# Kernel tuning notes

Hardware: AMD Instinct MI355X
Metric: run time of the kernel (lower is better)

## Reference

```python
import jax, jax.numpy as jnp
import numpy as np

RBF_CO = 10.077141124806595


def setup_inputs() -> dict:
    key = jax.random.key(0)
    k1, k2, k3 = jax.random.split(key, 3)
    n, dim = 2048, 128
    N, out_dim = 50000, 64
    features = jax.random.normal(k1, (n, dim), dtype=jnp.float32)
    train_data = jax.random.normal(k2, (N, dim), dtype=jnp.float32)
    weights = jax.random.normal(k3, (N, out_dim), dtype=jnp.float32) * 0.02
    return {"features": features, "train_data": train_data, "weights": weights}


def reference(features, train_data, weights):
    x2 = jnp.sum(features * features, axis=-1, keepdims=True)      # [n, 1]
    t2 = jnp.sum(train_data * train_data, axis=-1)                 # [N]
    d2 = x2 + t2[None, :] - 2.0 * (features @ train_data.T)        # [n, N]
    dist = jnp.sqrt(jnp.maximum(d2, 0.0))                          # clamp fp error
    k = jnp.exp(-dist / RBF_CO / 2.0)                              # RBF kernel [n, N]
    return k @ weights                                              # [n, out_dim]
```

## Files before the change

kernel.cpp:

```cpp
#include <hip/hip_runtime.h>
#include <hip/hip_bf16.h>
#include <stdint.h>

#define DIM 128
#define ODIM 64
#define BM 128
#define BN 64
#define NSPLIT 48
#define SPROW 72

typedef __attribute__((ext_vector_type(8))) __bf16 bf16x8;
typedef __attribute__((ext_vector_type(2))) __bf16 bf16x2;
typedef __attribute__((ext_vector_type(4))) float f32x4;

#define MFMA16(a, b, c) __builtin_amdgcn_mfma_f32_16x16x32_bf16((a), (b), (c), 0, 0, 0)

#define RBFD 10.077141124806595
#define LOG2E 1.4426950408889634
#define C2D ((LOG2E / (2.0 * RBFD)) * (LOG2E / (2.0 * RBFD)))

__device__ __forceinline__ void async_copy16(const void* g, void* l) {
  __builtin_amdgcn_global_load_lds((const __attribute__((address_space(1))) void*)g,
                                   (__attribute__((address_space(3))) void*)l, 16, 0, 0);
}
__device__ __forceinline__ void async_copy4(const void* g, void* l) {
  __builtin_amdgcn_global_load_lds((const __attribute__((address_space(1))) void*)g,
                                   (__attribute__((address_space(3))) void*)l, 4, 0, 0);
}

__device__ __forceinline__ uint32_t pack_bf16(float a, float b) {
  uint32_t ua = __builtin_bit_cast(uint32_t, a) + 0x8000u;
  uint32_t ub = __builtin_bit_cast(uint32_t, b) + 0x8000u;
  return __builtin_amdgcn_perm(ub, ua, 0x07060302u);
}

__global__ void prep_rows(const float* __restrict__ train, __bf16* __restrict__ Tb,
                          float* __restrict__ t2, const float* __restrict__ feat,
                          __bf16* __restrict__ Fb, float* __restrict__ x2,
                          int Ntrain, int NpadTrain, int nFeat, int trainBlocks, float scale) {
  int b = blockIdx.x;
  const float* src;
  __bf16* dst;
  float* sq;
  int nValid, nPad, row0;
  float padv;
  if (b < trainBlocks) {
    src = train; dst = Tb; sq = t2; nValid = Ntrain; nPad = NpadTrain; row0 = b * 4; padv = 1e30f;
  } else {
    src = feat; dst = Fb; sq = x2; nValid = nFeat; nPad = nFeat; row0 = (b - trainBlocks) * 4; padv = 0.0f;
  }
  int row = row0 + (threadIdx.x >> 6);
  int lane = threadIdx.x & 63;
  if (row >= nPad) return;
  float2 v = make_float2(0.0f, 0.0f);
  if (row < nValid) v = ((const float2*)src)[(size_t)row * 64 + lane];
  bf16x2 p;
  p.x = (__bf16)v.x;
  p.y = (__bf16)v.y;
  *(bf16x2*)&dst[(size_t)row * DIM + lane * 2] = p;
  float ss = v.x * v.x + v.y * v.y;
  #pragma unroll
  for (int off = 32; off > 0; off >>= 1) ss += __shfl_down(ss, off);
  if (lane == 0) sq[row] = (row < nValid) ? ss * scale : padv;
}

__global__ void transpose_weights(const float* __restrict__ W, __bf16* __restrict__ Wt,
                                  int N, int Npad) {
  __shared__ float tile[64][65];
  int j0 = (int)blockIdx.x * 64;
  int t = threadIdx.x;
  int jr = t >> 2;
  int cg = (t & 3) * 16;
  int j = j0 + jr;
  if (j < N) {
    const float4* src = (const float4*)(W + (size_t)j * ODIM);
    #pragma unroll
    for (int q = 0; q < 4; ++q) {
      float4 u = src[(cg >> 2) + q];
      tile[jr][cg + q * 4 + 0] = u.x;
      tile[jr][cg + q * 4 + 1] = u.y;
      tile[jr][cg + q * 4 + 2] = u.z;
      tile[jr][cg + q * 4 + 3] = u.w;
    }
  } else {
    #pragma unroll
    for (int q = 0; q < 16; ++q) tile[jr][cg + q] = 0.0f;
  }
  __syncthreads();
  int v = t >> 2;
  int jc = (t & 3) * 16;
  __bf16 ob[16];
  #pragma unroll
  for (int q = 0; q < 16; ++q) ob[q] = (__bf16)tile[jc + q][v];
  __bf16* dst = Wt + (size_t)v * Npad + j0 + jc;
  *(bf16x8*)dst = *(bf16x8*)&ob[0];
  *(bf16x8*)(dst + 8) = *(bf16x8*)&ob[8];
}

template <bool ATOMIC>
__global__ __launch_bounds__(256, 3) void rbf_main(
    const __bf16* __restrict__ Fb, const __bf16* __restrict__ Tb,
    const __bf16* __restrict__ Wt, const float* __restrict__ t2g,
    const float* __restrict__ x2g, float* __restrict__ outOrPart,
    int nRows, int Npad, int nChunks) {
  __shared__ __bf16 sT[BN * DIM];
  __shared__ __bf16 sW[ODIM * BN];
  __shared__ __bf16 sP[BM * SPROW];
  __shared__ float st2[BN];

  const int tid = threadIdx.x;
  const int wave = tid >> 6;
  const int lane = tid & 63;
  const int l16 = lane & 15;
  const int g4 = lane >> 4;

  const int ns = (int)blockIdx.x;
  const int mb = (int)blockIdx.y;

  constexpr float KNEG2 = (float)(-2.0 * C2D);

  bf16x8 bF[2][4];
  #pragma unroll
  for (int nf = 0; nf < 2; ++nf)
    #pragma unroll
    for (int ko = 0; ko < 4; ++ko)
      bF[nf][ko] = *(const bf16x8*)(Fb + ((size_t)(mb * BM + wave * 32 + nf * 16 + l16)) * DIM +
                                    ko * 32 + g4 * 8);

  float x2v[2];
  #pragma unroll
  for (int nf = 0; nf < 2; ++nf)
    x2v[nf] = x2g[mb * BM + wave * 32 + nf * 16 + l16];

  f32x4 zero4 = {0.0f, 0.0f, 0.0f, 0.0f};
  f32x4 oacc[2][4];
  #pragma unroll
  for (int mo = 0; mo < 2; ++mo)
    #pragma unroll
    for (int vi = 0; vi < 4; ++vi) oacc[mo][vi] = zero4;

  for (int c = ns; c < nChunks; c += NSPLIT) {
    const int n0 = c * BN;

    {
      const char* gT = (const char*)Tb + (size_t)n0 * 256;
      #pragma unroll
      for (int i = 0; i < 4; ++i) {
        int off = i * 4096 + wave * 1024;
        int loff = off + lane * 16;
        int row = loff >> 8;
        int gran = (loff >> 4) & 15;
        async_copy16(gT + row * 256 + ((gran ^ (row & 15)) << 4), (char*)sT + off);
      }
    }
    {
      #pragma unroll
      for (int i = 0; i < 2; ++i) {
        int off = i * 4096 + wave * 1024;
        int loff = off + lane * 16;
        int v = loff >> 7;
        int gran = (loff >> 4) & 7;
        const char* gW = (const char*)Wt + ((size_t)v * Npad + n0) * 2 + ((gran ^ (v & 7)) << 4);
        async_copy16(gW, (char*)sW + off);
      }
    }
    if (wave == 0) async_copy4((const char*)(t2g + n0) + lane * 4, (char*)st2);
    __syncthreads();

    f32x4 sacc[4][2];
    #pragma unroll
    for (int mt = 0; mt < 4; ++mt)
      #pragma unroll
      for (int nf = 0; nf < 2; ++nf) sacc[mt][nf] = zero4;

    #pragma unroll
    for (int ko = 0; ko < 4; ++ko) {
      bf16x8 a[4];
      #pragma unroll
      for (int mt = 0; mt < 4; ++mt) {
        int row = mt * 16 + l16;
        int slot = (ko * 4 + g4) ^ l16;
        a[mt] = *(const bf16x8*)((const char*)sT + row * 256 + (slot << 4));
      }
      #pragma unroll
      for (int mt = 0; mt < 4; ++mt)
        #pragma unroll
        for (int nf = 0; nf < 2; ++nf)
          sacc[mt][nf] = MFMA16(a[mt], bF[nf][ko], sacc[mt][nf]);
    }

    #pragma unroll
    for (int mt = 0; mt < 4; ++mt) {
      f32x4 t2v = *(const f32x4*)&st2[mt * 16 + g4 * 4];
      #pragma unroll
      for (int nf = 0; nf < 2; ++nf) {
        f32x4 s = sacc[mt][nf];
        float kv[4];
        #pragma unroll
        for (int r = 0; r < 4; ++r) {
          float d2 = __builtin_fmaf(KNEG2, s[r], t2v[r] + x2v[nf]);
          d2 = fmaxf(d2, 0.0f);
          kv[r] = __builtin_amdgcn_exp2f(-__builtin_amdgcn_sqrtf(d2));
        }
        uint32_t lo = pack_bf16(kv[0], kv[1]);
        uint32_t hi = pack_bf16(kv[2], kv[3]);
        uint2* dst = (uint2*)&sP[(wave * 32 + nf * 16 + l16) * SPROW + mt * 16 + g4 * 4];
        *dst = make_uint2(lo, hi);
      }
    }

    #pragma unroll
    for (int ko2 = 0; ko2 < 2; ++ko2) {
      bf16x8 p[2];
      #pragma unroll
      for (int mo = 0; mo < 2; ++mo)
        p[mo] = *(const bf16x8*)&sP[(wave * 32 + mo * 16 + l16) * SPROW + ko2 * 32 + g4 * 8];
      bf16x8 w[4];
      #pragma unroll
      for (int vi = 0; vi < 4; ++vi) {
        int v = vi * 16 + l16;
        int slot = (ko2 * 4 + g4) ^ (l16 & 7);
        w[vi] = *(const bf16x8*)((const char*)sW + v * 128 + (slot << 4));
      }
      #pragma unroll
      for (int mo = 0; mo < 2; ++mo)
        #pragma unroll
        for (int vi = 0; vi < 4; ++vi)
          oacc[mo][vi] = MFMA16(p[mo], w[vi], oacc[mo][vi]);
    }
    __syncthreads();
  }

  if (ATOMIC) {
    float* out = outOrPart;
    #pragma unroll
    for (int mo = 0; mo < 2; ++mo)
      #pragma unroll
      for (int vi = 0; vi < 4; ++vi)
        #pragma unroll
        for (int r = 0; r < 4; ++r) {
          int row = mb * BM + wave * 32 + mo * 16 + g4 * 4 + r;
          int col = vi * 16 + l16;
          atomicAdd(&out[(size_t)row * ODIM + col], oacc[mo][vi][r]);
        }
  } else {
    float* dst = outOrPart + (size_t)ns * (size_t)nRows * ODIM;
    #pragma unroll
    for (int mo = 0; mo < 2; ++mo)
      #pragma unroll
      for (int vi = 0; vi < 4; ++vi)
        #pragma unroll
        for (int r = 0; r < 4; ++r) {
          int row = mb * BM + wave * 32 + mo * 16 + g4 * 4 + r;
          int col = vi * 16 + l16;
          dst[(size_t)row * ODIM + col] = oacc[mo][vi][r];
        }
  }
}

__global__ void reduce_parts(const float4* __restrict__ part, float4* __restrict__ out,
                             int total4) {
  int i = (int)blockIdx.x * blockDim.x + threadIdx.x;
  if (i >= total4) return;
  float4 s = make_float4(0.0f, 0.0f, 0.0f, 0.0f);
  #pragma unroll
  for (int sp = 0; sp < NSPLIT; ++sp) {
    float4 v = part[(size_t)sp * total4 + i];
    s.x += v.x; s.y += v.y; s.z += v.z; s.w += v.w;
  }
  out[i] = s;
}

extern "C" void kernel_launch(void* const* d_in, const int* in_sizes, int n_in,
                              void* d_out, int out_size, void* d_ws, size_t ws_size,
                              hipStream_t stream) {
  (void)n_in;
  const float* features = (const float*)d_in[0];
  const float* train = (const float*)d_in[1];
  const float* weights = (const float*)d_in[2];
  float* out = (float*)d_out;

  const int n = in_sizes[0] / DIM;
  const int N = in_sizes[1] / DIM;
  const int Npad = ((N + 63) / 64) * 64;
  const int nChunks = Npad / 64;

  size_t off = 0;
  auto alloc = [&](size_t bytes) {
    size_t o = off;
    off = (off + bytes + 255) & ~(size_t)255;
    return o;
  };
  size_t oT = alloc((size_t)Npad * DIM * 2);
  size_t oW = alloc((size_t)ODIM * Npad * 2);
  size_t oF = alloc((size_t)n * DIM * 2);
  size_t ot2 = alloc((size_t)Npad * 4);
  size_t ox2 = alloc((size_t)n * 4);
  size_t oPart = alloc((size_t)NSPLIT * n * ODIM * 4);
  size_t needFull = off;

  char* ws = (char*)d_ws;
  __bf16* Tb = (__bf16*)(ws + oT);
  __bf16* Wt = (__bf16*)(ws + oW);
  __bf16* Fb = (__bf16*)(ws + oF);
  float* t2 = (float*)(ws + ot2);
  float* x2 = (float*)(ws + ox2);

  const float scale = (float)C2D;
  const int trainBlocks = Npad / 4;
  prep_rows<<<trainBlocks + n / 4, 256, 0, stream>>>(train, Tb, t2, features, Fb, x2,
                                                     N, Npad, n, trainBlocks, scale);
  transpose_weights<<<Npad / 64, 256, 0, stream>>>(weights, Wt, N, Npad);

  const int mBlocks = n / BM;
  dim3 grid(NSPLIT, mBlocks);

  if (ws_size >= needFull) {
    float* part = (float*)(ws + oPart);
    rbf_main<false><<<grid, 256, 0, stream>>>(Fb, Tb, Wt, t2, x2, part, n, Npad, nChunks);
    int total4 = n * ODIM / 4;
    reduce_parts<<<(total4 + 255) / 256, 256, 0, stream>>>((const float4*)part, (float4*)out,
                                                           total4);
  } else {
    hipMemsetAsync(d_out, 0, (size_t)out_size * sizeof(float), stream);
    rbf_main<true><<<grid, 256, 0, stream>>>(Fb, Tb, Wt, t2, x2, out, n, Npad, nChunks);
  }
}
```

Baseline: 147.9 us.

## Double-buffer tile loads, pass probabilities via lane swaps, fuse prep kernels

Double-buffers the train and weight tiles in LDS so the next chunk's async load is issued before the current chunk is computed, and drops one barrier per iteration. Rebuilds the RBF probability fragments for the second MFMA with permlane32/16 swaps instead of a round trip through an LDS staging buffer. Reads t2 straight from global memory, merges the two prep kernels into a single launch, and halves the reduce block size. This trades more LDS per block and extra cross-lane operations for fewer LDS round trips and better load/compute overlap. The single remaining barrier at the top of the loop may not fully protect the buffer being refilled.

```diff
diff --git a/kernel.cpp b/kernel.cpp
--- a/kernel.cpp
+++ b/kernel.cpp
@@ -7,11 +7,12 @@
 #define BM 128
 #define BN 64
 #define NSPLIT 48
-#define SPROW 72
 
 typedef __attribute__((ext_vector_type(8))) __bf16 bf16x8;
 typedef __attribute__((ext_vector_type(2))) __bf16 bf16x2;
 typedef __attribute__((ext_vector_type(4))) float f32x4;
+typedef __attribute__((ext_vector_type(2))) unsigned int uint32x2;
+typedef __attribute__((ext_vector_type(4))) unsigned int uint32x4;
 
 #define MFMA16(a, b, c) __builtin_amdgcn_mfma_f32_16x16x32_bf16((a), (b), (c), 0, 0, 0)
 
@@ -22,10 +23,6 @@
 __device__ __forceinline__ void async_copy16(const void* g, void* l) {
   __builtin_amdgcn_global_load_lds((const __attribute__((address_space(1))) void*)g,
                                    (__attribute__((address_space(3))) void*)l, 16, 0, 0);
-}
-__device__ __forceinline__ void async_copy4(const void* g, void* l) {
-  __builtin_amdgcn_global_load_lds((const __attribute__((address_space(1))) void*)g,
-                                   (__attribute__((address_space(3))) void*)l, 4, 0, 0);
 }
 
 __device__ __forceinline__ uint32_t pack_bf16(float a, float b) {
@@ -34,45 +31,48 @@
   return __builtin_amdgcn_perm(ub, ua, 0x07060302u);
 }
 
-__global__ void prep_rows(const float* __restrict__ train, __bf16* __restrict__ Tb,
-                          float* __restrict__ t2, const float* __restrict__ feat,
-                          __bf16* __restrict__ Fb, float* __restrict__ x2,
-                          int Ntrain, int NpadTrain, int nFeat, int trainBlocks, float scale) {
-  int b = blockIdx.x;
-  const float* src;
-  __bf16* dst;
-  float* sq;
-  int nValid, nPad, row0;
-  float padv;
-  if (b < trainBlocks) {
-    src = train; dst = Tb; sq = t2; nValid = Ntrain; nPad = NpadTrain; row0 = b * 4; padv = 1e30f;
-  } else {
-    src = feat; dst = Fb; sq = x2; nValid = nFeat; nPad = nFeat; row0 = (b - trainBlocks) * 4; padv = 0.0f;
-  }
-  int row = row0 + (threadIdx.x >> 6);
-  int lane = threadIdx.x & 63;
-  if (row >= nPad) return;
-  float2 v = make_float2(0.0f, 0.0f);
-  if (row < nValid) v = ((const float2*)src)[(size_t)row * 64 + lane];
-  bf16x2 p;
-  p.x = (__bf16)v.x;
-  p.y = (__bf16)v.y;
-  *(bf16x2*)&dst[(size_t)row * DIM + lane * 2] = p;
-  float ss = v.x * v.x + v.y * v.y;
-  #pragma unroll
-  for (int off = 32; off > 0; off >>= 1) ss += __shfl_down(ss, off);
-  if (lane == 0) sq[row] = (row < nValid) ? ss * scale : padv;
-}
-
-__global__ void transpose_weights(const float* __restrict__ W, __bf16* __restrict__ Wt,
-                                  int N, int Npad) {
+__global__ void prep_all(const float* __restrict__ train, __bf16* __restrict__ Tb,
+                         float* __restrict__ t2, const float* __restrict__ feat,
+                         __bf16* __restrict__ Fb, float* __restrict__ x2,
+                         const float* __restrict__ W, __bf16* __restrict__ Wt,
+                         int Ntrain, int Npad, int nFeat,
+                         int trainBlocks, int rowBlocks, float scale) {
   __shared__ float tile[64][65];
-  int j0 = (int)blockIdx.x * 64;
-  int t = threadIdx.x;
+  const int b = (int)blockIdx.x;
+  const int t = (int)threadIdx.x;
+
+  if (b < rowBlocks) {
+    const float* src;
+    __bf16* dst;
+    float* sq;
+    int nValid, nPad, row0;
+    float padv;
+    if (b < trainBlocks) {
+      src = train; dst = Tb; sq = t2; nValid = Ntrain; nPad = Npad; row0 = b * 4; padv = 1e30f;
+    } else {
+      src = feat; dst = Fb; sq = x2; nValid = nFeat; nPad = nFeat; row0 = (b - trainBlocks) * 4; padv = 0.0f;
+    }
+    int row = row0 + (t >> 6);
+    int lane = t & 63;
+    if (row >= nPad) return;
+    float2 v = make_float2(0.0f, 0.0f);
+    if (row < nValid) v = ((const float2*)src)[(size_t)row * 64 + lane];
+    bf16x2 p;
+    p.x = (__bf16)v.x;
+    p.y = (__bf16)v.y;
+    *(bf16x2*)&dst[(size_t)row * DIM + lane * 2] = p;
+    float ss = v.x * v.x + v.y * v.y;
+    #pragma unroll
+    for (int off = 32; off > 0; off >>= 1) ss += __shfl_down(ss, off);
+    if (lane == 0) sq[row] = (row < nValid) ? ss * scale : padv;
+    return;
+  }
+
+  int j0 = (b - rowBlocks) * 64;
   int jr = t >> 2;
   int cg = (t & 3) * 16;
   int j = j0 + jr;
-  if (j < N) {
+  if (j < Ntrain) {
     const float4* src = (const float4*)(W + (size_t)j * ODIM);
     #pragma unroll
     for (int q = 0; q < 4; ++q) {
@@ -103,10 +103,8 @@
     const __bf16* __restrict__ Wt, const float* __restrict__ t2g,
     const float* __restrict__ x2g, float* __restrict__ outOrPart,
     int nRows, int Npad, int nChunks) {
-  __shared__ __bf16 sT[BN * DIM];
-  __shared__ __bf16 sW[ODIM * BN];
-  __shared__ __bf16 sP[BM * SPROW];
-  __shared__ float st2[BN];
+  __shared__ __bf16 sT[2][BN * DIM];
+  __shared__ __bf16 sW[2][ODIM * BN];
 
   const int tid = threadIdx.x;
   const int wave = tid >> 6;
@@ -139,33 +137,43 @@
     #pragma unroll
     for (int vi = 0; vi < 4; ++vi) oacc[mo][vi] = zero4;
 
+  auto stage = [&](int bsel, int c) {
+    const char* gT = (const char*)Tb + (size_t)c * (BN * DIM * 2);
+    char* lT = (char*)&sT[bsel][0];
+    #pragma unroll
+    for (int i = 0; i < 4; ++i) {
+      int off = i * 4096 + wave * 1024;
+      int loff = off + lane * 16;
+      int row = loff >> 8;
+      int gran = (loff >> 4) & 15;
+      async_copy16(gT + row * 256 + ((gran ^ (row & 15)) << 4), lT + off);
+    }
+    char* lW = (char*)&sW[bsel][0];
+    #pragma unroll
+    for (int i = 0; i < 2; ++i) {
+      int off = i * 4096 + wave * 1024;
+      int loff = off + lane * 16;
+      int v = loff >> 7;
+      int gran = (loff >> 4) & 7;
+      const char* gW = (const char*)Wt + ((size_t)v * Npad + c * BN) * 2 + ((gran ^ (v & 7)) << 4);
+      async_copy16(gW, lW + off);
+    }
+  };
+
+  stage(0, ns);
+  int buf = 0;
+
   for (int c = ns; c < nChunks; c += NSPLIT) {
     const int n0 = c * BN;
-
-    {
-      const char* gT = (const char*)Tb + (size_t)n0 * 256;
-      #pragma unroll
-      for (int i = 0; i < 4; ++i) {
-        int off = i * 4096 + wave * 1024;
-        int loff = off + lane * 16;
-        int row = loff >> 8;
-        int gran = (loff >> 4) & 15;
-        async_copy16(gT + row * 256 + ((gran ^ (row & 15)) << 4), (char*)sT + off);
-      }
-    }
-    {
-      #pragma unroll
-      for (int i = 0; i < 2; ++i) {
-        int off = i * 4096 + wave * 1024;
-        int loff = off + lane * 16;
-        int v = loff >> 7;
-        int gran = (loff >> 4) & 7;
-        const char* gW = (const char*)Wt + ((size_t)v * Npad + n0) * 2 + ((gran ^ (v & 7)) << 4);
-        async_copy16(gW, (char*)sW + off);
-      }
-    }
-    if (wave == 0) async_copy4((const char*)(t2g + n0) + lane * 4, (char*)st2);
     __syncthreads();
+
+    f32x4 t2v[4];
+    #pragma unroll
+    for (int mt = 0; mt < 4; ++mt)
+      t2v[mt] = *(const f32x4*)(t2g + n0 + mt * 16 + g4 * 4);
+
+    int cn = c + NSPLIT;
+    if (cn < nChunks) stage(buf ^ 1, cn);
 
     f32x4 sacc[4][2];
     #pragma unroll
@@ -180,7 +188,7 @@
       for (int mt = 0; mt < 4; ++mt) {
         int row = mt * 16 + l16;
         int slot = (ko * 4 + g4) ^ l16;
-        a[mt] = *(const bf16x8*)((const char*)sT + row * 256 + (slot << 4));
+        a[mt] = *(const bf16x8*)((const char*)&sT[buf][0] + row * 256 + (slot << 4));
       }
       #pragma unroll
       for (int mt = 0; mt < 4; ++mt)
@@ -189,46 +197,50 @@
           sacc[mt][nf] = MFMA16(a[mt], bF[nf][ko], sacc[mt][nf]);
     }
 
+    uint32_t plo[4][2], phi[4][2];
     #pragma unroll
     for (int mt = 0; mt < 4; ++mt) {
-      f32x4 t2v = *(const f32x4*)&st2[mt * 16 + g4 * 4];
       #pragma unroll
       for (int nf = 0; nf < 2; ++nf) {
         f32x4 s = sacc[mt][nf];
         float kv[4];
         #pragma unroll
         for (int r = 0; r < 4; ++r) {
-          float d2 = __builtin_fmaf(KNEG2, s[r], t2v[r] + x2v[nf]);
+          float d2 = __builtin_fmaf(KNEG2, s[r], t2v[mt][r] + x2v[nf]);
           d2 = fmaxf(d2, 0.0f);
           kv[r] = __builtin_amdgcn_exp2f(-__builtin_amdgcn_sqrtf(d2));
         }
-        uint32_t lo = pack_bf16(kv[0], kv[1]);
-        uint32_t hi = pack_bf16(kv[2], kv[3]);
-        uint2* dst = (uint2*)&sP[(wave * 32 + nf * 16 + l16) * SPROW + mt * 16 + g4 * 4];
-        *dst = make_uint2(lo, hi);
+        plo[mt][nf] = pack_bf16(kv[0], kv[1]);
+        phi[mt][nf] = pack_bf16(kv[2], kv[3]);
       }
     }
 
     #pragma unroll
     for (int ko2 = 0; ko2 < 2; ++ko2) {
-      bf16x8 p[2];
-      #pragma unroll
-      for (int mo = 0; mo < 2; ++mo)
-        p[mo] = *(const bf16x8*)&sP[(wave * 32 + mo * 16 + l16) * SPROW + ko2 * 32 + g4 * 8];
       bf16x8 w[4];
       #pragma unroll
       for (int vi = 0; vi < 4; ++vi) {
         int v = vi * 16 + l16;
         int slot = (ko2 * 4 + g4) ^ (l16 & 7);
-        w[vi] = *(const bf16x8*)((const char*)sW + v * 128 + (slot << 4));
+        w[vi] = *(const bf16x8*)((const char*)&sW[buf][0] + v * 128 + (slot << 4));
       }
       #pragma unroll
-      for (int mo = 0; mo < 2; ++mo)
+      for (int nf = 0; nf < 2; ++nf) {
+        uint32x2 rA = __builtin_amdgcn_permlane32_swap(plo[2 * ko2][nf], plo[2 * ko2 + 1][nf],
+                                                       false, false);
+        uint32x2 rB = __builtin_amdgcn_permlane16_swap(rA[0], rA[1], false, false);
+        uint32x2 rC = __builtin_amdgcn_permlane32_swap(phi[2 * ko2][nf], phi[2 * ko2 + 1][nf],
+                                                       false, false);
+        uint32x2 rD = __builtin_amdgcn_permlane16_swap(rC[0], rC[1], false, false);
+        uint32x4 pd = {rB[0], rD[0], rB[1], rD[1]};
+        bf16x8 p = __builtin_bit_cast(bf16x8, pd);
         #pragma unroll
         for (int vi = 0; vi < 4; ++vi)
-          oacc[mo][vi] = MFMA16(p[mo], w[vi], oacc[mo][vi]);
-    }
-    __syncthreads();
+          oacc[nf][vi] = MFMA16(p, w[vi], oacc[nf][vi]);
+      }
+    }
+
+    buf ^= 1;
   }
 
   if (ATOMIC) {
@@ -308,9 +320,11 @@
 
   const float scale = (float)C2D;
   const int trainBlocks = Npad / 4;
-  prep_rows<<<trainBlocks + n / 4, 256, 0, stream>>>(train, Tb, t2, features, Fb, x2,
-                                                     N, Npad, n, trainBlocks, scale);
-  transpose_weights<<<Npad / 64, 256, 0, stream>>>(weights, Wt, N, Npad);
+  const int rowBlocks = trainBlocks + n / 4;
+  const int wBlocks = Npad / 64;
+  prep_all<<<rowBlocks + wBlocks, 256, 0, stream>>>(train, Tb, t2, features, Fb, x2,
+                                                    weights, Wt, N, Npad, n,
+                                                    trainBlocks, rowBlocks, scale);
 
   const int mBlocks = n / BM;
   dim3 grid(NSPLIT, mBlocks);
@@ -319,7 +333,7 @@
     float* part = (float*)(ws + oPart);
     rbf_main<false><<<grid, 256, 0, stream>>>(Fb, Tb, Wt, t2, x2, part, n, Npad, nChunks);
     int total4 = n * ODIM / 4;
-    reduce_parts<<<(total4 + 255) / 256, 256, 0, stream>>>((const float4*)part, (float4*)out,
+    reduce_parts<<<(total4 + 127) / 128, 128, 0, stream>>>((const float4*)part, (float4*)out,
                                                            total4);
   } else {
     hipMemsetAsync(d_out, 0, (size_t)out_size * sizeof(float), stream);
```

New measurement: 150.8 us. About the same (+2.0%).

## Fuse prep kernels, fold distance scaling into inputs, swizzle P tile in LDS

Applied to the files above, without the earlier changes.

Merges the row-prep and weight-transpose kernels into a single launch. The -2*C2D factor is folded into the bf16 train data, and the MFMA accumulators are seeded with t2+x2, which removes the per-element FMA in the epilogue. t2 is now loaded straight from global memory into registers instead of going through LDS. The padded P tile is replaced by an XOR-swizzled 64-column layout to cut LDS footprint. Scaling train by -2*C2D before the bf16 cast changes rounding slightly, and the extra register-held t2 values raise register pressure.

```diff
diff --git a/kernel.cpp b/kernel.cpp
--- a/kernel.cpp
+++ b/kernel.cpp
@@ -7,7 +7,6 @@
 #define BM 128
 #define BN 64
 #define NSPLIT 48
-#define SPROW 72
 
 typedef __attribute__((ext_vector_type(8))) __bf16 bf16x8;
 typedef __attribute__((ext_vector_type(2))) __bf16 bf16x2;
@@ -22,10 +21,6 @@
 __device__ __forceinline__ void async_copy16(const void* g, void* l) {
   __builtin_amdgcn_global_load_lds((const __attribute__((address_space(1))) void*)g,
                                    (__attribute__((address_space(3))) void*)l, 16, 0, 0);
-}
-__device__ __forceinline__ void async_copy4(const void* g, void* l) {
-  __builtin_amdgcn_global_load_lds((const __attribute__((address_space(1))) void*)g,
-                                   (__attribute__((address_space(3))) void*)l, 4, 0, 0);
 }
 
 __device__ __forceinline__ uint32_t pack_bf16(float a, float b) {
@@ -34,45 +29,50 @@
   return __builtin_amdgcn_perm(ub, ua, 0x07060302u);
 }
 
-__global__ void prep_rows(const float* __restrict__ train, __bf16* __restrict__ Tb,
-                          float* __restrict__ t2, const float* __restrict__ feat,
-                          __bf16* __restrict__ Fb, float* __restrict__ x2,
-                          int Ntrain, int NpadTrain, int nFeat, int trainBlocks, float scale) {
-  int b = blockIdx.x;
-  const float* src;
-  __bf16* dst;
-  float* sq;
-  int nValid, nPad, row0;
-  float padv;
-  if (b < trainBlocks) {
-    src = train; dst = Tb; sq = t2; nValid = Ntrain; nPad = NpadTrain; row0 = b * 4; padv = 1e30f;
-  } else {
-    src = feat; dst = Fb; sq = x2; nValid = nFeat; nPad = nFeat; row0 = (b - trainBlocks) * 4; padv = 0.0f;
-  }
-  int row = row0 + (threadIdx.x >> 6);
-  int lane = threadIdx.x & 63;
-  if (row >= nPad) return;
-  float2 v = make_float2(0.0f, 0.0f);
-  if (row < nValid) v = ((const float2*)src)[(size_t)row * 64 + lane];
-  bf16x2 p;
-  p.x = (__bf16)v.x;
-  p.y = (__bf16)v.y;
-  *(bf16x2*)&dst[(size_t)row * DIM + lane * 2] = p;
-  float ss = v.x * v.x + v.y * v.y;
-  #pragma unroll
-  for (int off = 32; off > 0; off >>= 1) ss += __shfl_down(ss, off);
-  if (lane == 0) sq[row] = (row < nValid) ? ss * scale : padv;
-}
-
-__global__ void transpose_weights(const float* __restrict__ W, __bf16* __restrict__ Wt,
-                                  int N, int Npad) {
+__global__ void prep_all(const float* __restrict__ train, __bf16* __restrict__ Tb,
+                         float* __restrict__ t2, const float* __restrict__ feat,
+                         __bf16* __restrict__ Fb, float* __restrict__ x2,
+                         const float* __restrict__ W, __bf16* __restrict__ Wt,
+                         int Ntrain, int Npad, int nFeat,
+                         int trainBlocks, int rowBlocks, float scale, float tScale) {
   __shared__ float tile[64][65];
-  int j0 = (int)blockIdx.x * 64;
-  int t = threadIdx.x;
+  const int b = (int)blockIdx.x;
+  const int t = (int)threadIdx.x;
+
+  if (b < rowBlocks) {
+    const float* src;
+    __bf16* dst;
+    float* sq;
+    int nValid, nPad, row0;
+    float padv, rowScale;
+    if (b < trainBlocks) {
+      src = train; dst = Tb; sq = t2; nValid = Ntrain; nPad = Npad; row0 = b * 4;
+      padv = 1e30f; rowScale = tScale;
+    } else {
+      src = feat; dst = Fb; sq = x2; nValid = nFeat; nPad = nFeat; row0 = (b - trainBlocks) * 4;
+      padv = 0.0f; rowScale = 1.0f;
+    }
+    int row = row0 + (t >> 6);
+    int lane = t & 63;
+    if (row >= nPad) return;
+    float2 v = make_float2(0.0f, 0.0f);
+    if (row < nValid) v = ((const float2*)src)[(size_t)row * 64 + lane];
+    float ss = v.x * v.x + v.y * v.y;
+    bf16x2 p;
+    p.x = (__bf16)(v.x * rowScale);
+    p.y = (__bf16)(v.y * rowScale);
+    *(bf16x2*)&dst[(size_t)row * DIM + lane * 2] = p;
+    #pragma unroll
+    for (int off = 32; off > 0; off >>= 1) ss += __shfl_down(ss, off);
+    if (lane == 0) sq[row] = (row < nValid) ? ss * scale : padv;
+    return;
+  }
+
+  int j0 = (b - rowBlocks) * 64;
   int jr = t >> 2;
   int cg = (t & 3) * 16;
   int j = j0 + jr;
-  if (j < N) {
+  if (j < Ntrain) {
     const float4* src = (const float4*)(W + (size_t)j * ODIM);
     #pragma unroll
     for (int q = 0; q < 4; ++q) {
@@ -105,8 +105,7 @@
     int nRows, int Npad, int nChunks) {
   __shared__ __bf16 sT[BN * DIM];
   __shared__ __bf16 sW[ODIM * BN];
-  __shared__ __bf16 sP[BM * SPROW];
-  __shared__ float st2[BN];
+  __shared__ __bf16 sP[BM * 64];
 
   const int tid = threadIdx.x;
   const int wave = tid >> 6;
@@ -116,8 +115,6 @@
 
   const int ns = (int)blockIdx.x;
   const int mb = (int)blockIdx.y;
-
-  constexpr float KNEG2 = (float)(-2.0 * C2D);
 
   bf16x8 bF[2][4];
   #pragma unroll
@@ -164,14 +161,20 @@
         async_copy16(gW, (char*)sW + off);
       }
     }
-    if (wave == 0) async_copy4((const char*)(t2g + n0) + lane * 4, (char*)st2);
+    f32x4 t2v[4];
+    #pragma unroll
+    for (int mt = 0; mt < 4; ++mt)
+      t2v[mt] = *(const f32x4*)(t2g + n0 + mt * 16 + g4 * 4);
+
     __syncthreads();
 
     f32x4 sacc[4][2];
     #pragma unroll
     for (int mt = 0; mt < 4; ++mt)
       #pragma unroll
-      for (int nf = 0; nf < 2; ++nf) sacc[mt][nf] = zero4;
+      for (int nf = 0; nf < 2; ++nf)
+        #pragma unroll
+        for (int r = 0; r < 4; ++r) sacc[mt][nf][r] = t2v[mt][r] + x2v[nf];
 
     #pragma unroll
     for (int ko = 0; ko < 4; ++ko) {
@@ -191,20 +194,19 @@
 
     #pragma unroll
     for (int mt = 0; mt < 4; ++mt) {
-      f32x4 t2v = *(const f32x4*)&st2[mt * 16 + g4 * 4];
       #pragma unroll
       for (int nf = 0; nf < 2; ++nf) {
-        f32x4 s = sacc[mt][nf];
         float kv[4];
         #pragma unroll
         for (int r = 0; r < 4; ++r) {
-          float d2 = __builtin_fmaf(KNEG2, s[r], t2v[r] + x2v[nf]);
-          d2 = fmaxf(d2, 0.0f);
+          float d2 = fmaxf(sacc[mt][nf][r], 0.0f);
           kv[r] = __builtin_amdgcn_exp2f(-__builtin_amdgcn_sqrtf(d2));
         }
         uint32_t lo = pack_bf16(kv[0], kv[1]);
         uint32_t hi = pack_bf16(kv[2], kv[3]);
-        uint2* dst = (uint2*)&sP[(wave * 32 + nf * 16 + l16) * SPROW + mt * 16 + g4 * 4];
+        int prow = wave * 32 + nf * 16 + l16;
+        int gran = (2 * mt + (g4 >> 1)) ^ (l16 & 7);
+        uint2* dst = (uint2*)((char*)sP + prow * 128 + (gran << 4) + (g4 & 1) * 8);
         *dst = make_uint2(lo, hi);
       }
     }
@@ -213,8 +215,11 @@
     for (int ko2 = 0; ko2 < 2; ++ko2) {
       bf16x8 p[2];
       #pragma unroll
-      for (int mo = 0; mo < 2; ++mo)
-        p[mo] = *(const bf16x8*)&sP[(wave * 32 + mo * 16 + l16) * SPROW + ko2 * 32 + g4 * 8];
+      for (int mo = 0; mo < 2; ++mo) {
+        int prow = wave * 32 + mo * 16 + l16;
+        int gran = (ko2 * 4 + g4) ^ (l16 & 7);
+        p[mo] = *(const bf16x8*)((const char*)sP + prow * 128 + (gran << 4));
+      }
       bf16x8 w[4];
       #pragma unroll
       for (int vi = 0; vi < 4; ++vi) {
@@ -307,10 +312,13 @@
   float* x2 = (float*)(ws + ox2);
 
   const float scale = (float)C2D;
+  const float tScale = (float)(-2.0 * C2D);
   const int trainBlocks = Npad / 4;
-  prep_rows<<<trainBlocks + n / 4, 256, 0, stream>>>(train, Tb, t2, features, Fb, x2,
-                                                     N, Npad, n, trainBlocks, scale);
-  transpose_weights<<<Npad / 64, 256, 0, stream>>>(weights, Wt, N, Npad);
+  const int rowBlocks = trainBlocks + n / 4;
+  const int wBlocks = Npad / 64;
+  prep_all<<<rowBlocks + wBlocks, 256, 0, stream>>>(train, Tb, t2, features, Fb, x2,
+                                                    weights, Wt, N, Npad, n,
+                                                    trainBlocks, rowBlocks, scale, tScale);
 
   const int mBlocks = n / BM;
   dim3 grid(NSPLIT, mBlocks);
```

New measurement: 146.6 us. About the same (-0.8%).
